# Performance work log

Hardware: AMD Instinct MI355X
Metric: run time of the kernel (lower is better)

The kernel has to match this reference:

```python
import jax, jax.numpy as jnp
import numpy as np

LOGIT_SCALE = 1.0
REDUCTION = "mean"

N, H, V = 4096, 512, 50257


def setup_inputs() -> dict:
    key = jax.random.key(0)
    k1, k2, k3, k4 = jax.random.split(key, 4)
    x = jax.random.normal(k1, (N, H), dtype=jnp.float32)
    targets = jax.random.normal(k2, (N, V), dtype=jnp.float32)
    weight = jax.random.normal(k3, (V, H), dtype=jnp.float32) * 0.02
    bias = jax.random.normal(k4, (V,), dtype=jnp.float32) * 0.02
    return {"x": x, "targets": targets, "weight": weight, "bias": bias}


def reference(x, targets, weight, bias):
    # logits = x @ W^T + b  -> [N, V]
    logits = jnp.einsum("nh,vh->nv", x, weight) + bias
    scaled = logits * LOGIT_SCALE
    # logsumexp over vocab for both predicted and target logits (fp32)
    lse_logits = jax.nn.logsumexp(scaled, axis=-1)                      # [N]
    lse_targets = jax.nn.logsumexp(targets, axis=-1)                    # [N]
    # original: .nan_to_num(nan=inf) -> rows with nan targets contribute 0
    lse_targets = jnp.where(jnp.isnan(lse_targets), jnp.inf, lse_targets)
    p_target = jnp.exp(targets - lse_targets[:, None])                  # softmax(targets)
    log_p_pred = scaled - lse_logits[:, None]                           # log_softmax(scaled logits)
    per_row_loss = -jnp.sum(p_target * log_p_pred, axis=-1)             # [N]
    loss = per_row_loss.sum()
    if REDUCTION == "mean":
        loss = loss / N
    return loss
```

## Files before the change

kernel.cpp:

```cpp
#include <hip/hip_runtime.h>
#include <hip/hip_bf16.h>

#define N_ROWS 4096
#define H_DIM  512
#define V_DIM  50257
#define BM 128
#define BN 128
#define BK 64
#define NSTEP (H_DIM / BK)
#define VT_TOTAL 393
#define V_PAD (VT_TOTAL * BN)
#define NCHUNK 131
#define LOG2E 1.4426950408889634f
#define BUF0 0
#define BUF1 32768

typedef __attribute__((ext_vector_type(8))) short short8;
typedef __attribute__((ext_vector_type(4))) float f32x4;

static __device__ __forceinline__ unsigned short f2bf(float f) {
  unsigned u = __float_as_uint(f);
  u = (u + 0x7fffu + ((u >> 16) & 1u)) >> 16;
  return (unsigned short)u;
}

static __device__ __forceinline__ void gload_lds16(const void* g, void* l) {
  __builtin_amdgcn_global_load_lds(
      (const __attribute__((address_space(1))) void*)g,
      (__attribute__((address_space(3))) void*)l, 16, 0, 0);
}

__global__ void convert_kernel(const float* __restrict__ X,
                               const float* __restrict__ W,
                               __hip_bfloat16* __restrict__ Xb,
                               __hip_bfloat16* __restrict__ Wb) {
  const long wtot8 = (long)V_PAD * H_DIM / 8;
  const long xtot8 = (long)N_ROWS * H_DIM / 8;
  long i = (long)blockIdx.x * blockDim.x + threadIdx.x;
  unsigned short o[8];
  if (i < wtot8) {
    long base = i * 8;
    long row = base >> 9;
    if (row < V_DIM) {
      const float4* s = (const float4*)(W + base);
      float4 a = s[0], b = s[1];
      o[0]=f2bf(a.x); o[1]=f2bf(a.y); o[2]=f2bf(a.z); o[3]=f2bf(a.w);
      o[4]=f2bf(b.x); o[5]=f2bf(b.y); o[6]=f2bf(b.z); o[7]=f2bf(b.w);
    } else {
      #pragma unroll
      for (int k = 0; k < 8; ++k) o[k] = 0;
    }
    *(short8*)(Wb + base) = *(const short8*)o;
  } else if (i < wtot8 + xtot8) {
    long base = (i - wtot8) * 8;
    const float4* s = (const float4*)(X + base);
    float4 a = s[0], b = s[1];
    o[0]=f2bf(a.x); o[1]=f2bf(a.y); o[2]=f2bf(a.z); o[3]=f2bf(a.w);
    o[4]=f2bf(b.x); o[5]=f2bf(b.y); o[6]=f2bf(b.z); o[7]=f2bf(b.w);
    *(short8*)(Xb + base) = *(const short8*)o;
  }
}

template <bool GUARD>
static __device__ __forceinline__ void chunk_stats(
    const f32x4 (&T)[4], const f32x4 (&L)[4], int gcol0,
    float& mlr, float& slr, float& mtr, float& str, float& ddr) {
  float Lv[16], Tv[16];
  #pragma unroll
  for (int c = 0; c < 4; ++c)
    #pragma unroll
    for (int j = 0; j < 4; ++j) {
      const int k = c * 4 + j;
      const bool ok = !GUARD || (gcol0 + c * 4 + j < V_DIM);
      Lv[k] = ok ? L[c][j] : -1e30f;
      Tv[k] = ok ? T[c][j] : -1e30f;
    }
  float g = Lv[0];
  #pragma unroll
  for (int k = 1; k < 16; ++k) g = fmaxf(g, Lv[k]);
  if (g > mlr + 12.f) { slr *= exp2f((mlr - g) * LOG2E); mlr = g; }
  float bl = mlr * LOG2E;
  float ss = 0.f;
  #pragma unroll
  for (int k = 0; k < 16; ++k) ss += exp2f(__builtin_fmaf(Lv[k], LOG2E, -bl));
  slr += ss;
  float gt = Tv[0];
  #pragma unroll
  for (int k = 1; k < 16; ++k) gt = fmaxf(gt, Tv[k]);
  if (gt > mtr + 12.f) {
    float sc = exp2f((mtr - gt) * LOG2E);
    str *= sc; ddr *= sc; mtr = gt;
  }
  float bt = mtr * LOG2E;
  float s2 = 0.f, d2 = 0.f;
  #pragma unroll
  for (int k = 0; k < 16; ++k) {
    float e = exp2f(__builtin_fmaf(Tv[k], LOG2E, -bt));
    s2 += e;
    d2 = __builtin_fmaf(e, Lv[k], d2);
  }
  str += s2; ddr += d2;
}

template <bool GUARD>
static __device__ __forceinline__ void stream_tile(
    const float* __restrict__ targets, const char* __restrict__ Lrow,
    long growVD, int vbase, int cb0, int rsw, long tlim,
    float& mlr, float& slr, float& mtr, float& str, float& ddr) {
  f32x4 T0[4], T1[4], L[4];
  auto LOADT = [&](f32x4 (&D)[4], int i) {
    #pragma unroll
    for (int c = 0; c < 4; ++c) {
      long off = growVD + vbase + cb0 + i * 16 + c * 4;
      if (GUARD) off = off > tlim ? tlim : off;
      D[c] = *(const f32x4*)(targets + off);
    }
  };
  auto LOADL = [&](int i) {
    #pragma unroll
    for (int c = 0; c < 4; ++c)
      L[c] = *(const f32x4*)(Lrow + (((cb0 + i * 16 + c * 4) * 4) ^ rsw));
  };
  LOADT(T0, 0); LOADT(T1, 1);
  LOADL(0); chunk_stats<GUARD>(T0, L, vbase + cb0 +  0, mlr, slr, mtr, str, ddr);
  LOADT(T0, 2);
  LOADL(1); chunk_stats<GUARD>(T1, L, vbase + cb0 + 16, mlr, slr, mtr, str, ddr);
  LOADT(T1, 3);
  LOADL(2); chunk_stats<GUARD>(T0, L, vbase + cb0 + 32, mlr, slr, mtr, str, ddr);
  LOADL(3); chunk_stats<GUARD>(T1, L, vbase + cb0 + 48, mlr, slr, mtr, str, ddr);
}

__global__ __launch_bounds__(256, 2)
void fused_kernel(const __hip_bfloat16* __restrict__ Xb,
                  const __hip_bfloat16* __restrict__ Wb,
                  const float* __restrict__ bias,
                  const float* __restrict__ targets,
                  float* __restrict__ partials) {
  __shared__ __align__(16) char smem[65536];

  const int tid  = threadIdx.x;
  const int lane = tid & 63;
  const int wid  = tid >> 6;
  const int wm   = wid >> 1;
  const int wn   = wid & 1;
  const int q    = lane >> 4;
  const int c15  = lane & 15;
  const int brow = blockIdx.x;
  const int chunk = blockIdx.y;

  float mlr = -1e30f, slr = 0.f, mtr = -1e30f, str = 0.f, ddr = 0.f;

  const int srow8 = tid >> 3;
  const int soff  = ((tid & 7) * 8) ^ ((srow8 & 7) * 8);
  const __hip_bfloat16* asrc = Xb + (long)(brow * BM + srow8) * H_DIM + soff;

  const int rm      = (c15 & 7) << 4;
  const int arow_b  = (wm * 64 + c15) * 128;
  const int brow_b  = (wn * 64 + c15) * 128;

  auto stage = [&](int bufb, const __hip_bfloat16* a_s,
                   const __hip_bfloat16* b_s, int kk) {
    #pragma unroll
    for (int i = 0; i < 4; ++i)
      gload_lds16(a_s + (long)i * 32 * H_DIM + kk,
                  smem + bufb + i * 4096 + tid * 16);
    #pragma unroll
    for (int i = 0; i < 4; ++i)
      gload_lds16(b_s + (long)i * 32 * H_DIM + kk,
                  smem + bufb + 16384 + i * 4096 + tid * 16);
  };

  const int srow  = tid >> 1;
  const int shalf = tid & 1;
  const int cb0   = shalf * 64;
  const long grow   = (long)(brow * BM + srow);
  const long growVD = grow * V_DIM;
  const long tlim   = (long)N_ROWS * V_DIM - 4;
  const char* Lrow  = smem + srow * 512;
  const int rsw     = (srow & 7) << 4;

  #pragma unroll 1
  for (int vt = chunk; vt < VT_TOTAL; vt += NCHUNK) {
    const int vbase = vt * BN;
    const int v0 = vbase + wn * 64 + q * 4;

    const __hip_bfloat16* bsrc = Wb + (long)(vbase + srow8) * H_DIM + soff;
    stage(BUF0, asrc, bsrc, 0);
    __syncthreads();

    f32x4 acc[4][4];
    #pragma unroll
    for (int a = 0; a < 4; ++a)
      #pragma unroll
      for (int b = 0; b < 4; ++b)
        acc[a][b] = (f32x4){0.f, 0.f, 0.f, 0.f};

    #pragma unroll
    for (int ks = 0; ks < NSTEP; ++ks) {
      const int cb = (ks & 1) ? BUF1 : BUF0;
      const int nb = (ks & 1) ? BUF0 : BUF1;
      if (ks < NSTEP - 1)
        stage(nb, asrc, bsrc, (ks + 1) * BK);

      #pragma unroll
      for (int s = 0; s < 2; ++s) {
        short8 xf[4], wf[4];
        #pragma unroll
        for (int a = 0; a < 4; ++a)
          xf[a] = *(const short8*)(smem + cb + arow_b + a * 2048 +
                                   ((s * 64 + q * 16) ^ rm));
        #pragma unroll
        for (int b = 0; b < 4; ++b)
          wf[b] = *(const short8*)(smem + cb + 16384 + brow_b + b * 2048 +
                                   ((s * 64 + q * 16) ^ rm));
        #pragma unroll
        for (int a = 0; a < 4; ++a)
          #pragma unroll
          for (int b = 0; b < 4; ++b)
            acc[a][b] = __builtin_amdgcn_mfma_f32_16x16x32_bf16(
                wf[b], xf[a], acc[a][b], 0, 0, 0);
      }
      __syncthreads();
    }

    f32x4 bp[4];
    #pragma unroll
    for (int b = 0; b < 4; ++b) {
      int bo = v0 + b * 16;
      bo = bo > (V_DIM - 4) ? (V_DIM - 4) : bo;
      bp[b] = *(const f32x4*)(bias + bo);
    }
    #pragma unroll
    for (int a = 0; a < 4; ++a) {
      const int row = wm * 64 + a * 16 + c15;
      char* rbase = smem + row * 512;
      #pragma unroll
      for (int b = 0; b < 4; ++b) {
        f32x4 v;
        #pragma unroll
        for (int j = 0; j < 4; ++j) v[j] = acc[a][b][j] + bp[b][j];
        *(f32x4*)(rbase + ((wn * 256 + b * 64 + q * 16) ^ rm)) = v;
      }
    }
    __syncthreads();

    if (vt == VT_TOTAL - 1)
      stream_tile<true >(targets, Lrow, growVD, vbase, cb0, rsw, tlim,
                         mlr, slr, mtr, str, ddr);
    else
      stream_tile<false>(targets, Lrow, growVD, vbase, cb0, rsw, tlim,
                         mlr, slr, mtr, str, ddr);
    __syncthreads();
  }

  {
    float ml2 = __shfl_xor(mlr, 1);
    float sl2 = __shfl_xor(slr, 1);
    float mt2 = __shfl_xor(mtr, 1);
    float st2 = __shfl_xor(str, 1);
    float dd2 = __shfl_xor(ddr, 1);
    float nm = fmaxf(mlr, ml2);
    float slo = slr * exp2f((mlr - nm) * LOG2E) + sl2 * exp2f((ml2 - nm) * LOG2E);
    float nmt = fmaxf(mtr, mt2);
    float e1 = exp2f((mtr - nmt) * LOG2E);
    float e2 = exp2f((mt2 - nmt) * LOG2E);
    float sto = str * e1 + st2 * e2;
    float ddo = ddr * e1 + dd2 * e2;
    if (shalf == 0) {
      float* o = partials + (grow * NCHUNK + chunk) * 5;
      o[0] = nm; o[1] = slo; o[2] = nmt; o[3] = sto; o[4] = ddo;
    }
  }
}

__global__ void rowloss_kernel(const float* __restrict__ partials,
                               float* __restrict__ rowloss) {
  int r = blockIdx.x * blockDim.x + threadIdx.x;
  if (r >= N_ROWS) return;
  const float* p = partials + (long)r * NCHUNK * 5;
  float ml = -1e30f, sl = 0.f, mt = -1e30f, st = 0.f, dd = 0.f;
  for (int c = 0; c < NCHUNK; ++c) {
    float ml2 = p[0], sl2 = p[1], mt2 = p[2], st2 = p[3], dd2 = p[4];
    p += 5;
    float nm = fmaxf(ml, ml2);
    sl = sl * exp2f((ml - nm) * LOG2E) + sl2 * exp2f((ml2 - nm) * LOG2E);
    ml = nm;
    float nmt = fmaxf(mt, mt2);
    float e1 = exp2f((mt - nmt) * LOG2E);
    float e2 = exp2f((mt2 - nmt) * LOG2E);
    st = st * e1 + st2 * e2;
    dd = dd * e1 + dd2 * e2;
    mt = nmt;
  }
  float lse = ml + logf(sl);
  rowloss[r] = lse - dd / st;
}

__global__ void final_kernel(const float* __restrict__ rowloss,
                             float* __restrict__ out) {
  __shared__ float sm[4];
  float s = 0.f;
  for (int i = threadIdx.x; i < N_ROWS; i += 256) s += rowloss[i];
  #pragma unroll
  for (int off = 32; off > 0; off >>= 1) s += __shfl_down(s, off);
  if ((threadIdx.x & 63) == 0) sm[threadIdx.x >> 6] = s;
  __syncthreads();
  if (threadIdx.x == 0) out[0] = (sm[0] + sm[1] + sm[2] + sm[3]) * (1.0f / (float)N_ROWS);
}

extern "C" void kernel_launch(void* const* d_in, const int* in_sizes, int n_in,
                              void* d_out, int out_size, void* d_ws, size_t ws_size,
                              hipStream_t stream) {
  const float* x       = (const float*)d_in[0];
  const float* targets = (const float*)d_in[1];
  const float* weight  = (const float*)d_in[2];
  const float* bias    = (const float*)d_in[3];
  float* out = (float*)d_out;

  char* ws = (char*)d_ws;
  __hip_bfloat16* Wb = (__hip_bfloat16*)ws;
  size_t off = (size_t)V_PAD * H_DIM * 2;
  __hip_bfloat16* Xb = (__hip_bfloat16*)(ws + off);
  off += (size_t)N_ROWS * H_DIM * 2;
  float* partials = (float*)(ws + off);
  off += (size_t)N_ROWS * NCHUNK * 5 * sizeof(float);
  float* rowloss = (float*)(ws + off);

  convert_kernel<<<13600, 256, 0, stream>>>(x, weight, Xb, Wb);
  dim3 grid(N_ROWS / BM, NCHUNK);
  fused_kernel<<<grid, 256, 0, stream>>>(Xb, Wb, bias, targets, partials);
  rowloss_kernel<<<N_ROWS / 256, 256, 0, stream>>>(partials, rowloss);
  final_kernel<<<1, 256, 0, stream>>>(rowloss, out);
}
```

Measured before the change: 520.5 us.

## Prefetch next vocab tile's first K-slice across tiles; store logits as bf16 in LDS

The first K-step staging of the next vocab tile is now issued during the last K-step of the current tile. The logits staging area moves to a separate LDS region so the prefetch does not collide with it. __syncthreads is replaced by explicit vmcnt/lgkmcnt waits plus raw barriers, and MFMA sections are wrapped in s_setprio. Logits are rounded to bf16 before being written to LDS, which halves LDS traffic and footprint but loses precision in the logsumexp and cross term.

Result: slower. 558.1 us (+7.2%).

```diff
diff --git a/kernel.cpp b/kernel.cpp
--- a/kernel.cpp
+++ b/kernel.cpp
@@ -14,6 +14,12 @@
 #define LOG2E 1.4426950408889634f
 #define BUF0 0
 #define BUF1 32768
+#define LBASE 32768
+
+#define VMCNT8() asm volatile("s_waitcnt vmcnt(8)" ::: "memory")
+#define VMCNT0() asm volatile("s_waitcnt vmcnt(0)" ::: "memory")
+#define LGKM0()  asm volatile("s_waitcnt lgkmcnt(0)" ::: "memory")
+#define BARRIER() __builtin_amdgcn_s_barrier()
 
 typedef __attribute__((ext_vector_type(8))) short short8;
 typedef __attribute__((ext_vector_type(4))) float f32x4;
@@ -63,18 +69,15 @@
 
 template <bool GUARD>
 static __device__ __forceinline__ void chunk_stats(
-    const f32x4 (&T)[4], const f32x4 (&L)[4], int gcol0,
+    const float (&Lraw)[16], const f32x4 (&T)[4], int gcol0,
     float& mlr, float& slr, float& mtr, float& str, float& ddr) {
   float Lv[16], Tv[16];
   #pragma unroll
-  for (int c = 0; c < 4; ++c)
-    #pragma unroll
-    for (int j = 0; j < 4; ++j) {
-      const int k = c * 4 + j;
-      const bool ok = !GUARD || (gcol0 + c * 4 + j < V_DIM);
-      Lv[k] = ok ? L[c][j] : -1e30f;
-      Tv[k] = ok ? T[c][j] : -1e30f;
-    }
+  for (int k = 0; k < 16; ++k) {
+    const bool ok = !GUARD || (gcol0 + k < V_DIM);
+    Lv[k] = ok ? Lraw[k] : -1e30f;
+    Tv[k] = ok ? T[k >> 2][k & 3] : -1e30f;
+  }
   float g = Lv[0];
   #pragma unroll
   for (int k = 1; k < 16; ++k) g = fmaxf(g, Lv[k]);
@@ -107,7 +110,7 @@
     const float* __restrict__ targets, const char* __restrict__ Lrow,
     long growVD, int vbase, int cb0, int rsw, long tlim,
     float& mlr, float& slr, float& mtr, float& str, float& ddr) {
-  f32x4 T0[4], T1[4], L[4];
+  f32x4 T0[4], T1[4];
   auto LOADT = [&](f32x4 (&D)[4], int i) {
     #pragma unroll
     for (int c = 0; c < 4; ++c) {
@@ -116,18 +119,25 @@
       D[c] = *(const f32x4*)(targets + off);
     }
   };
-  auto LOADL = [&](int i) {
-    #pragma unroll
-    for (int c = 0; c < 4; ++c)
-      L[c] = *(const f32x4*)(Lrow + (((cb0 + i * 16 + c * 4) * 4) ^ rsw));
+  auto DOCHUNK = [&](const f32x4 (&T)[4], int i) {
+    const int ob = (cb0 << 1) + (i << 5);
+    short8 l0 = *(const short8*)(Lrow + ((ob) ^ rsw));
+    short8 l1 = *(const short8*)(Lrow + ((ob + 16) ^ rsw));
+    float Lraw[16];
+    #pragma unroll
+    for (int e = 0; e < 8; ++e) {
+      Lraw[e]     = __uint_as_float(((unsigned)(unsigned short)l0[e]) << 16);
+      Lraw[e + 8] = __uint_as_float(((unsigned)(unsigned short)l1[e]) << 16);
+    }
+    chunk_stats<GUARD>(Lraw, T, vbase + cb0 + i * 16, mlr, slr, mtr, str, ddr);
   };
   LOADT(T0, 0); LOADT(T1, 1);
-  LOADL(0); chunk_stats<GUARD>(T0, L, vbase + cb0 +  0, mlr, slr, mtr, str, ddr);
+  DOCHUNK(T0, 0);
   LOADT(T0, 2);
-  LOADL(1); chunk_stats<GUARD>(T1, L, vbase + cb0 + 16, mlr, slr, mtr, str, ddr);
+  DOCHUNK(T1, 1);
   LOADT(T1, 3);
-  LOADL(2); chunk_stats<GUARD>(T0, L, vbase + cb0 + 32, mlr, slr, mtr, str, ddr);
-  LOADL(3); chunk_stats<GUARD>(T1, L, vbase + cb0 + 48, mlr, slr, mtr, str, ddr);
+  DOCHUNK(T0, 2);
+  DOCHUNK(T1, 3);
 }
 
 __global__ __launch_bounds__(256, 2)
@@ -176,17 +186,19 @@
   const long grow   = (long)(brow * BM + srow);
   const long growVD = grow * V_DIM;
   const long tlim   = (long)N_ROWS * V_DIM - 4;
-  const char* Lrow  = smem + srow * 512;
+  const char* Lrow  = smem + LBASE + srow * 256;
   const int rsw     = (srow & 7) << 4;
+
+  const __hip_bfloat16* bsrc = Wb + (long)(chunk * BN + srow8) * H_DIM + soff;
+  stage(BUF0, asrc, bsrc, 0);
 
   #pragma unroll 1
   for (int vt = chunk; vt < VT_TOTAL; vt += NCHUNK) {
     const int vbase = vt * BN;
     const int v0 = vbase + wn * 64 + q * 4;
-
-    const __hip_bfloat16* bsrc = Wb + (long)(vbase + srow8) * H_DIM + soff;
-    stage(BUF0, asrc, bsrc, 0);
-    __syncthreads();
+    const bool last = (vt + NCHUNK >= VT_TOTAL);
+    const __hip_bfloat16* bsrc_next =
+        Wb + (long)((vt + NCHUNK) * BN + srow8) * H_DIM + soff;
 
     f32x4 acc[4][4];
     #pragma unroll
@@ -198,9 +210,14 @@
     #pragma unroll
     for (int ks = 0; ks < NSTEP; ++ks) {
       const int cb = (ks & 1) ? BUF1 : BUF0;
-      const int nb = (ks & 1) ? BUF0 : BUF1;
+      const int nb = cb ^ 32768;
       if (ks < NSTEP - 1)
         stage(nb, asrc, bsrc, (ks + 1) * BK);
+      else if (!last)
+        stage(nb, asrc, bsrc_next, 0);
+
+      if (ks == NSTEP - 1 && last) { VMCNT0(); } else { VMCNT8(); }
+      BARRIER();
 
       #pragma unroll
       for (int s = 0; s < 2; ++s) {
@@ -213,15 +230,19 @@
         for (int b = 0; b < 4; ++b)
           wf[b] = *(const short8*)(smem + cb + 16384 + brow_b + b * 2048 +
                                    ((s * 64 + q * 16) ^ rm));
+        __builtin_amdgcn_s_setprio(1);
         #pragma unroll
         for (int a = 0; a < 4; ++a)
           #pragma unroll
           for (int b = 0; b < 4; ++b)
             acc[a][b] = __builtin_amdgcn_mfma_f32_16x16x32_bf16(
                 wf[b], xf[a], acc[a][b], 0, 0, 0);
+        __builtin_amdgcn_s_setprio(0);
       }
-      __syncthreads();
-    }
+      LGKM0();
+      BARRIER();
+    }
+    bsrc = bsrc_next;
 
     f32x4 bp[4];
     #pragma unroll
@@ -233,16 +254,20 @@
     #pragma unroll
     for (int a = 0; a < 4; ++a) {
       const int row = wm * 64 + a * 16 + c15;
-      char* rbase = smem + row * 512;
+      char* rb = smem + LBASE + row * 256;
       #pragma unroll
       for (int b = 0; b < 4; ++b) {
-        f32x4 v;
-        #pragma unroll
-        for (int j = 0; j < 4; ++j) v[j] = acc[a][b][j] + bp[b][j];
-        *(f32x4*)(rbase + ((wn * 256 + b * 64 + q * 16) ^ rm)) = v;
+        uint2 w;
+        w.x = (unsigned)f2bf(acc[a][b][0] + bp[b][0]) |
+              ((unsigned)f2bf(acc[a][b][1] + bp[b][1]) << 16);
+        w.y = (unsigned)f2bf(acc[a][b][2] + bp[b][2]) |
+              ((unsigned)f2bf(acc[a][b][3] + bp[b][3]) << 16);
+        const int o = wn * 128 + b * 32 + q * 8;
+        *(uint2*)(rb + (o ^ rm)) = w;
       }
     }
-    __syncthreads();
+    LGKM0();
+    BARRIER();
 
     if (vt == VT_TOTAL - 1)
       stream_tile<true >(targets, Lrow, growVD, vbase, cb0, rsw, tlim,
@@ -250,7 +275,8 @@
     else
       stream_tile<false>(targets, Lrow, growVD, vbase, cb0, rsw, tlim,
                          mlr, slr, mtr, str, ddr);
-    __syncthreads();
+    LGKM0();
+    BARRIER();
   }
 
   {
```
